# Kernel optimization log

Hardware: AMD Instinct MI355X
Metric: run time of the kernel (lower is better)

The kernel has to match this reference:

```python
import jax, jax.numpy as jnp
import numpy as np

B, S, E, P, H, F = 4, 4096, 256, 32, 8, 1024
DH = E // H
LN_EPS = 1e-5


def setup_inputs() -> dict:
    key = jax.random.key(0)
    ks = jax.random.split(key, 12)
    dt = jnp.float32
    return {
        "src": jax.random.normal(ks[0], (B, S, E), dt),
        "pos_embed": jax.random.normal(ks[1], (B, P, S), dt),
        # learnable positional transform (pos_linear: P -> P)
        "Wpos": jax.random.normal(ks[2], (P, P), dt) * (1.0 / np.sqrt(P)),
        "bpos": jnp.zeros((P,), dt),
        # RBF kernel hyperparameters (ScaleKernel(RBFKernel)) -- positive scalars
        "lengthscale": jnp.full((), 2.0, dt),
        "outputscale": jnp.full((), 1.0, dt),
        # value / output projections of multihead attention
        "Wv": jax.random.normal(ks[3], (E, E), dt) * (1.0 / np.sqrt(E)),
        "bv": jnp.zeros((E,), dt),
        "Wo": jax.random.normal(ks[4], (E, E), dt) * (1.0 / np.sqrt(E)),
        "bo": jnp.zeros((E,), dt),
        # feed-forward
        "W1": jax.random.normal(ks[5], (F, E), dt) * (1.0 / np.sqrt(E)),
        "b1": jnp.zeros((F,), dt),
        "W2": jax.random.normal(ks[6], (E, F), dt) * (1.0 / np.sqrt(F)),
        "b2": jnp.zeros((E,), dt),
        # layer norms
        "ln1_g": jnp.ones((E,), dt), "ln1_b": jnp.zeros((E,), dt),
        "ln2_g": jnp.ones((E,), dt), "ln2_b": jnp.zeros((E,), dt),
    }


def _layer_norm(x, g, b):
    mu = jnp.mean(x, -1, keepdims=True)
    var = jnp.mean(jnp.square(x - mu), -1, keepdims=True)
    return (x - mu) * jax.lax.rsqrt(var + LN_EPS) * g + b


def _rbf_scores(x, lengthscale, outputscale):
    # x: [B, S, P] -> scaled RBF kernel matrix [B, S, S]
    xs = x / lengthscale
    sq = jnp.sum(xs * xs, axis=-1)  # [B, S]
    d2 = sq[:, :, None] + sq[:, None, :] - 2.0 * jnp.einsum('bsp,btp->bst', xs, xs)
    d2 = jnp.maximum(d2, 0.0)
    return outputscale * jnp.exp(-0.5 * d2)


def reference(src, pos_embed, Wpos, bpos, lengthscale, outputscale,
              Wv, bv, Wo, bo, W1, b1, W2, b2, ln1_g, ln1_b, ln2_g, ln2_b):
    b, s, e = src.shape
    # learnable positional transform: [B,P,S] -> [B,S,P] -> linear -> back
    pe = jnp.einsum('bps,op->bos', pos_embed, Wpos) + bpos[None, :, None]  # [B,P,S]
    # GP-kernel attention scores over sequence positions
    scores = _rbf_scores(pe.transpose(0, 2, 1), lengthscale, outputscale)  # [B,S,S]
    attn = jax.nn.softmax(scores, axis=-1)
    # value projection, per-head weighted sum (scores shared across heads)
    v = (src @ Wv.T + bv).reshape(b, s, H, DH)
    ctx = jnp.einsum('bqk,bkhd->bqhd', attn, v).reshape(b, s, e)
    attn_out = ctx @ Wo.T + bo
    x = _layer_norm(src + attn_out, ln1_g, ln1_b)
    ff = jax.nn.relu(x @ W1.T + b1) @ W2.T + b2
    return _layer_norm(x + ff, ln2_g, ln2_b)
```

## Files before the change

### kernel.cpp

```cpp
#include <hip/hip_runtime.h>
#include <stdint.h>

#define BN 4
#define SN 4096
#define EN 256
#define PN 32
#define FN 1024
#define BS (BN*SN)
#define PAUG 64

typedef uint16_t bf16_t;
typedef short v4s  __attribute__((ext_vector_type(4)));
typedef short v8s  __attribute__((ext_vector_type(8)));
typedef __bf16 bf16x8 __attribute__((ext_vector_type(8)));
typedef float v4f   __attribute__((ext_vector_type(4)));
typedef float v16f  __attribute__((ext_vector_type(16)));

#define MFMA16(a,b,c) __builtin_amdgcn_mfma_f32_16x16x32_bf16(a,b,c,0,0,0)
#define MFMA32(a,b,c) __builtin_amdgcn_mfma_f32_32x32x16_bf16(a,b,c,0,0,0)

__device__ __forceinline__ float b2f(bf16_t x){
    uint32_t u = ((uint32_t)x) << 16; float f; __builtin_memcpy(&f, &u, 4); return f;
}
__device__ __forceinline__ bf16_t f2b(float f){
    uint32_t u; __builtin_memcpy(&u, &f, 4);
    u += 0x7FFFu + ((u >> 16) & 1u);
    return (bf16_t)(u >> 16);
}
__device__ __forceinline__ bf16x8 ldb8(const bf16_t* p){
    v8s r = *(const v8s*)p; return __builtin_bit_cast(bf16x8, r);
}
__device__ __forceinline__ bf16x8 ldb8u(const bf16_t* p){
    v4s lo = *(const v4s*)p;
    v4s hi = *(const v4s*)(p + 4);
    v8s r = __builtin_shufflevector(lo, hi, 0,1,2,3,4,5,6,7);
    return __builtin_bit_cast(bf16x8, r);
}
__device__ __forceinline__ float ldsc(const float* p){ return *p; }
__device__ __forceinline__ float ldsc(const bf16_t* p){ return b2f(*p); }
__device__ __forceinline__ void stsc(float* p, float v){ *p = v; }
__device__ __forceinline__ void stsc(bf16_t* p, float v){ *p = f2b(v); }

#if __has_builtin(__builtin_amdgcn_exp2f)
__device__ __forceinline__ float fexp2(float x){ return __builtin_amdgcn_exp2f(x); }
#else
__device__ __forceinline__ float fexp2(float x){ return exp2f(x); }
#endif

#if __has_builtin(__builtin_amdgcn_cvt_pk_bf16_f32)
typedef __bf16 bf16x2 __attribute__((ext_vector_type(2)));
__device__ __forceinline__ uint32_t pkbf16(float a, float b){
    bf16x2 r = __builtin_amdgcn_cvt_pk_bf16_f32(a, b);
    return __builtin_bit_cast(uint32_t, r);
}
#else
__device__ __forceinline__ uint32_t pkbf16(float a, float b){
    return (uint32_t)f2b(a) | ((uint32_t)f2b(b) << 16);
}
#endif

typedef const __attribute__((address_space(1))) uint32_t* glds_gp;
typedef __attribute__((address_space(3))) uint32_t* glds_lp;
__device__ __forceinline__ void glds16(const bf16_t* g, bf16_t* l){
    __builtin_amdgcn_global_load_lds((glds_gp)g, (glds_lp)l, 16, 0, 0);
}

__global__ __launch_bounds__(256) void prep_kernel(
    const float* __restrict__ src, bf16_t* __restrict__ srcb,
    const float* __restrict__ Wv, bf16_t* __restrict__ Wvb,
    const float* __restrict__ Wo, bf16_t* __restrict__ Wob,
    const float* __restrict__ W1, bf16_t* __restrict__ W1b,
    const float* __restrict__ W2, bf16_t* __restrict__ W2b,
    const float* __restrict__ pos, const float* __restrict__ Wp,
    const float* __restrict__ bp,  const float* __restrict__ lsp,
    bf16_t* __restrict__ xk, bf16_t* __restrict__ xq)
{
    __shared__ float Wsh[PN*PN];
    __shared__ float bsh[PN];
    int bid = blockIdx.x;
    int tid = threadIdx.x;

    if (bid < 4736){
        const float* sp; bf16_t* dp; int off;
        if (bid < 4096){ sp = src; dp = srcb; off = (bid*256 + tid)*4; }
        else {
            int i = ((bid - 4096)*256 + tid)*4;
            if      (i <  65536){ sp=Wv; dp=Wvb; off=i; }
            else if (i < 131072){
                int idx = i - 65536;
                float4 f = *(const float4*)(Wo + idx);
                v4s o;
                o.x = (short)f2b(f.x); o.y = (short)f2b(f.y);
                o.z = (short)f2b(f.z); o.w = (short)f2b(f.w);
                int n = idx >> 8, k = idx & 255;
                int dst = (((n>>4)*8 + (k>>5))*64 + (((k>>3)&3)*16 + (n&15)))*8 + (k&7);
                *(v4s*)(Wob + dst) = o;
                return;
            }
            else if (i < 393216){ sp=W1; dp=W1b; off=i-131072; }
            else                { sp=W2; dp=W2b; off=i-393216; }
        }
        float4 f = *(const float4*)(sp + off);
        v4s o;
        o.x = (short)f2b(f.x); o.y = (short)f2b(f.y);
        o.z = (short)f2b(f.z); o.w = (short)f2b(f.w);
        *(v4s*)(dp + off) = o;
        return;
    }

    int pb = bid - 4736;
    int b  = pb >> 4;
    int s  = (pb & 15)*256 + tid;

    for (int i = tid; i < PN*PN; i += 256) Wsh[i] = Wp[i];
    if (tid < PN) bsh[tid] = bp[tid];
    __syncthreads();

    float inv_ls = 1.0f / lsp[0];
    const float c1f = 1.4426950408889634f;

    float col[PN];
    #pragma unroll
    for (int p = 0; p < PN; p++) col[p] = pos[((size_t)b*PN + p)*SN + s];

    uint16_t xb[PN], qb[PN];
    float sq = 0.f;
    #pragma unroll 4
    for (int o = 0; o < PN; o++){
        float pe = bsh[o];
        #pragma unroll
        for (int p = 0; p < PN; p++) pe += col[p] * Wsh[o*PN + p];
        float pv = pe * inv_ls;
        uint16_t h = f2b(pv);
        xb[o] = h;
        qb[o] = f2b(c1f * pv);
        float xr = b2f(h);
        sq += xr * xr;
    }

    size_t base = ((size_t)b*SN + s) * PAUG;
    v8s pk[8];
    #pragma unroll
    for (int c = 0; c < 4; c++)
        #pragma unroll
        for (int j = 0; j < 8; j++) ((short*)&pk[c])[j] = (short)xb[c*8 + j];
    #pragma unroll
    for (int c = 4; c < 8; c++)
        #pragma unroll
        for (int j = 0; j < 8; j++) ((short*)&pk[c])[j] = 0;
    ((short*)&pk[4])[0] = (short)f2b(-0.5f * sq);
    ((short*)&pk[4])[1] = (short)0x3F80;
    #pragma unroll
    for (int c = 0; c < 8; c++) *(v8s*)(xk + base + c*8) = pk[c];

    #pragma unroll
    for (int c = 0; c < 4; c++)
        #pragma unroll
        for (int j = 0; j < 8; j++) ((short*)&pk[c])[j] = (short)qb[c*8 + j];
    ((short*)&pk[4])[0] = (short)f2b(c1f);
    ((short*)&pk[4])[1] = (short)f2b(-0.5f * sq * c1f);
    #pragma unroll
    for (int c = 0; c < 8; c++) *(v8s*)(xq + base + c*8) = pk[c];
}

template<int EPI, typename OutT>
__global__ __launch_bounds__(256) void gemm_t(
    const bf16_t* __restrict__ A, const bf16_t* __restrict__ W,
    const float* __restrict__ bias, OutT* __restrict__ out,
    bf16_t* __restrict__ vt, int N, int K)
{
    __shared__ __align__(16) bf16_t At[2][4096];
    __shared__ __align__(16) bf16_t Wt[2][4096];
    int tid = threadIdx.x;
    int lane = tid & 63, wv = tid >> 6, col = lane & 15, quad = lane >> 4;
    int m0 = blockIdx.x * 64, n0 = blockIdx.y * 64;
    int nck = K >> 6;

    int srow = tid >> 3;
    int spc  = (tid & 7) ^ (srow & 7);
    const bf16_t* asrc = A + (size_t)(m0 + srow)*K + spc*8;
    const bf16_t* wsrc = W + (size_t)(n0 + srow)*K + spc*8;

    v4f acc[4];
    #pragma unroll
    for (int t = 0; t < 4; t++) acc[t] = (v4f){0.f,0.f,0.f,0.f};

    glds16(asrc, &At[0][tid*8]);
    glds16(asrc + (size_t)32*K, &At[0][2048 + tid*8]);
    glds16(wsrc, &Wt[0][tid*8]);
    glds16(wsrc + (size_t)32*K, &Wt[0][2048 + tid*8]);
    __syncthreads();

    for (int c = 0; c < nck; c++){
        int cb = c & 1;
        if (c + 1 < nck){
            glds16(asrc + (c+1)*64, &At[cb^1][tid*8]);
            glds16(asrc + (size_t)32*K + (c+1)*64, &At[cb^1][2048 + tid*8]);
            glds16(wsrc + (c+1)*64, &Wt[cb^1][tid*8]);
            glds16(wsrc + (size_t)32*K + (c+1)*64, &Wt[cb^1][2048 + tid*8]);
        }
        #pragma unroll
        for (int kc = 0; kc < 2; kc++){
            int pc = ((kc*4 + quad) ^ (col & 7)) * 8;
            bf16x8 a = ldb8(&At[cb][(wv*16 + col)*64 + pc]);
            #pragma unroll
            for (int t = 0; t < 4; t++){
                bf16x8 b = ldb8(&Wt[cb][(t*16 + col)*64 + pc]);
                acc[t] = MFMA16(a, b, acc[t]);
            }
        }
        __syncthreads();
    }

    float bfv[4];
    #pragma unroll
    for (int t = 0; t < 4; t++) bfv[t] = bias[n0 + t*16 + col];

    if constexpr (EPI == 3){
        __shared__ uint16_t Tsh[64*74];
        #pragma unroll
        for (int r = 0; r < 4; r++)
            #pragma unroll
            for (int t = 0; t < 4; t++)
                Tsh[(wv*16 + quad*4 + r)*74 + t*16 + col] = f2b(acc[t][r] + bfv[t]);
        __syncthreads();
        int e = tid & 63, sc = tid >> 6;
        int b = m0 >> 12;
        int sbat = m0 & (SN-1);
        int eb   = (n0 + e) >> 5;
        int l31e = (n0 + e) & 31;
        int k16  = (sbat >> 4) + sc;
        v8s p0, p1;
        #pragma unroll
        for (int i = 0; i < 8; i++) ((short*)&p0)[i] = (short)Tsh[(sc*16 + i)*74 + e];
        #pragma unroll
        for (int i = 0; i < 8; i++) ((short*)&p1)[i] = (short)Tsh[(sc*16 + 8 + i)*74 + e];
        bf16_t* dst = vt + ((((size_t)b*8 + eb)*256 + k16)*64 + l31e)*8;
        *(v8s*)dst = p0;
        *(v8s*)(dst + 256) = p1;
    } else {
        #pragma unroll
        for (int r = 0; r < 4; r++){
            int row = m0 + wv*16 + quad*4 + r;
            #pragma unroll
            for (int t = 0; t < 4; t++){
                float y = acc[t][r] + bfv[t];
                if constexpr (EPI == 1) y = fmaxf(y, 0.f);
                stsc(out + (size_t)row*N + n0 + t*16 + col, y);
            }
        }
    }
}

__global__ __launch_bounds__(512) void ffn_ln_kernel(
    const bf16_t* __restrict__ x,  const bf16_t* __restrict__ W1b,
    const float* __restrict__ b1,  const bf16_t* __restrict__ W2b,
    const float* __restrict__ b2,  const float* __restrict__ gamma,
    const float* __restrict__ beta, float* __restrict__ out)
{
    __shared__ __align__(16) bf16_t W1c[2][16384];
    __shared__ __align__(16) bf16_t W2c[2][16384];
    __shared__ __align__(16) bf16_t Hs[64*68];
    __shared__ float b1sh[1024];
    __shared__ float lnb[2][64][2];

    int tid  = threadIdx.x;
    int lane = tid & 63;
    int wv   = tid >> 6;
    int col  = lane & 15;
    int quad = lane >> 4;
    int mw   = wv >> 1;
    int nw   = wv & 1;
    int m0   = blockIdx.x * 64;

    b1sh[tid]       = b1[tid];
    b1sh[512 + tid] = b1[512 + tid];

    const bf16_t* xrow = x + (size_t)(m0 + mw*16 + col)*EN + quad*8;
    bf16x8 xr[8];
    #pragma unroll
    for (int kk = 0; kk < 8; kk++) xr[kk] = ldb8(xrow + kk*32);

    float b2v[8], gv[8], bev[8];
    #pragma unroll
    for (int t2 = 0; t2 < 8; t2++){
        int nn = nw*128 + t2*16 + col;
        b2v[t2] = b2[nn]; gv[t2] = gamma[nn]; bev[t2] = beta[nn];
    }

    v4f acc[8];
    #pragma unroll
    for (int t2 = 0; t2 < 8; t2++) acc[t2] = (v4f){0.f,0.f,0.f,0.f};

    int wr  = tid >> 3;
    int pp  = tid & 7;
    int swz = (pp ^ (wr & 7)) * 8;

    #pragma unroll
    for (int s = 0; s < 4; s++)
        glds16(W1b + (size_t)wr*256 + s*64 + swz, &W1c[0][s*4096 + tid*8]);
    #pragma unroll
    for (int s2 = 0; s2 < 4; s2++)
        glds16(W2b + (size_t)(s2*64 + wr)*1024 + swz, &W2c[0][s2*4096 + tid*8]);

    #pragma unroll 1
    for (int c = 0; c < 16; c++){
        int par = c & 1;
        if (c < 15){
            #pragma unroll
            for (int s = 0; s < 4; s++)
                glds16(W1b + (size_t)((c+1)*64 + wr)*256 + s*64 + swz,
                       &W1c[par^1][s*4096 + tid*8]);
            #pragma unroll
            for (int s2 = 0; s2 < 4; s2++)
                glds16(W2b + (size_t)(s2*64 + wr)*1024 + (c+1)*64 + swz,
                       &W2c[par^1][s2*4096 + tid*8]);
            asm volatile("s_waitcnt vmcnt(8)" ::: "memory");
        } else {
            asm volatile("s_waitcnt vmcnt(0)" ::: "memory");
        }
        __builtin_amdgcn_s_barrier();
        __builtin_amdgcn_sched_barrier(0);

        v4f hacc[2];
        hacc[0] = (v4f){0.f,0.f,0.f,0.f};
        hacc[1] = (v4f){0.f,0.f,0.f,0.f};
        #pragma unroll
        for (int kk = 0; kk < 8; kk++){
            #pragma unroll
            for (int t = 0; t < 2; t++){
                int hl = nw*32 + t*16 + col;
                bf16x8 b = ldb8(&W1c[par][(kk>>1)*4096 + hl*64
                                 + ((((kk&1)*4 + quad) ^ (hl & 7))*8)]);
                hacc[t] = MFMA16(xr[kk], b, hacc[t]);
            }
        }
        #pragma unroll
        for (int t = 0; t < 2; t++){
            float bb = b1sh[c*64 + nw*32 + t*16 + col];
            #pragma unroll
            for (int r = 0; r < 4; r++){
                float h = fmaxf(hacc[t][r] + bb, 0.f);
                Hs[(mw*16 + quad*4 + r)*68 + nw*32 + t*16 + col] = f2b(h);
            }
        }
        asm volatile("s_waitcnt lgkmcnt(0)" ::: "memory");
        __builtin_amdgcn_s_barrier();
        __builtin_amdgcn_sched_barrier(0);

        #pragma unroll
        for (int kk2 = 0; kk2 < 2; kk2++){
            bf16x8 a2 = ldb8u(&Hs[(mw*16 + col)*68 + kk2*32 + quad*8]);
            #pragma unroll
            for (int t2 = 0; t2 < 8; t2++){
                int nn = nw*128 + t2*16 + col;
                bf16x8 bfr = ldb8(&W2c[par][(nn>>6)*4096 + (nn&63)*64
                                  + ((((kk2*4 + quad) ^ (col & 7)))*8)]);
                acc[t2] = MFMA16(a2, bfr, acc[t2]);
            }
        }
        asm volatile("s_waitcnt lgkmcnt(0)" ::: "memory");
        __builtin_amdgcn_s_barrier();
    }

    float v[8][4];
    float s1[4], s2[4];
    #pragma unroll
    for (int r = 0; r < 4; r++){ s1[r] = 0.f; s2[r] = 0.f; }
    #pragma unroll
    for (int r = 0; r < 4; r++){
        int row = m0 + mw*16 + quad*4 + r;
        #pragma unroll
        for (int t2 = 0; t2 < 8; t2++){
            int nn = nw*128 + t2*16 + col;
            float xv = acc[t2][r] + b2v[t2] + b2f(x[(size_t)row*EN + nn]);
            v[t2][r] = xv; s1[r] += xv; s2[r] += xv*xv;
        }
    }
    #pragma unroll
    for (int r = 0; r < 4; r++){
        #pragma unroll
        for (int m = 1; m <= 8; m <<= 1){
            s1[r] += __shfl_xor(s1[r], m);
            s2[r] += __shfl_xor(s2[r], m);
        }
    }
    if (col == 0){
        #pragma unroll
        for (int r = 0; r < 4; r++){
            int rl = mw*16 + quad*4 + r;
            lnb[nw][rl][0] = s1[r];
            lnb[nw][rl][1] = s2[r];
        }
    }
    __syncthreads();
    #pragma unroll
    for (int r = 0; r < 4; r++){
        int rl  = mw*16 + quad*4 + r;
        int row = m0 + rl;
        float S1 = lnb[0][rl][0] + lnb[1][rl][0];
        float S2 = lnb[0][rl][1] + lnb[1][rl][1];
        float mu = S1 * (1.f/256.f);
        float rs = rsqrtf(S2 * (1.f/256.f) - mu*mu + 1e-5f);
        #pragma unroll
        for (int t2 = 0; t2 < 8; t2++){
            int nn = nw*128 + t2*16 + col;
            out[(size_t)row*EN + nn] = (v[t2][r] - mu)*rs*gv[t2] + bev[t2];
        }
    }
}

__global__ __launch_bounds__(512, 2) void attn_kernel(
    const bf16_t* __restrict__ xk, const bf16_t* __restrict__ xq,
    const bf16_t* __restrict__ vf, const float* __restrict__ osp,
    const bf16_t* __restrict__ wof, const float* __restrict__ bo,
    const bf16_t* __restrict__ res, const float* __restrict__ gamma,
    const float* __restrict__ beta, bf16_t* __restrict__ out)
{
    __shared__ __align__(16) bf16_t Wtb[2][64*260];
    __shared__ __align__(16) bf16_t Qs[64*64];
    __shared__ __align__(16) bf16_t Osh[64*256];
    __shared__ float densh[8][64];
    __shared__ float dent[64];
    __shared__ float lnw[8][64][2];

    int tid  = threadIdx.x;
    int lane = tid & 63;
    int wv   = tid >> 6;
    int col  = lane & 15;
    int quad = lane >> 4;
    int l31  = lane & 31;
    int half = lane >> 5;

    int bid = blockIdx.x;
    int b   = (bid & 7) >> 1;
    int qi  = ((bid >> 3) << 1) | (bid & 1);
    int q0  = qi * 64;

    float k2 = 1.4426950408889634f * osp[0];

    const bf16_t* xkb = xk + (size_t)b * SN * PAUG;
    const bf16_t* xqb = xq + (size_t)b * SN * PAUG;
    const bf16_t* vfb = vf + (((size_t)b*8 + wv)*256)*512 + lane*8;

    {
        int qrow = tid >> 3;
        int qpc  = (tid & 7) ^ (qrow & 7);
        glds16(xqb + (size_t)(q0 + qrow)*PAUG + qpc*8, &Qs[tid*8]);
    }

    v16f acc[2];
    #pragma unroll
    for (int qg = 0; qg < 2; qg++)
        #pragma unroll
        for (int i = 0; i < 16; i++) acc[qg][i] = 0.f;
    float den[4] = {0.f, 0.f, 0.f, 0.f};
    const v4f zero = (v4f){0.f,0.f,0.f,0.f};

    bf16x8 kf[2][2];
    #pragma unroll
    for (int kg = 0; kg < 2; kg++)
        #pragma unroll
        for (int h = 0; h < 2; h++)
            kf[kg][h] = ldb8(xkb + (size_t)(wv*32 + kg*16 + col)*PAUG + h*32 + quad*8);

    __syncthreads();

    for (int c = 0; c < 16; c++){
        int cb = c & 1;
        bf16x8 vr[16];
        #pragma unroll
        for (int sk = 0; sk < 16; sk++)
            vr[sk] = ldb8(vfb + (size_t)(c*16 + sk)*512);

        #pragma unroll
        for (int qg = 0; qg < 2; qg++){
            #pragma unroll
            for (int g2 = 0; g2 < 2; g2++){
                int qr = qg*32 + g2*16 + col;
                bf16x8 qa = ldb8(&Qs[qr*64 + ((quad    ) ^ (col & 7))*8]);
                bf16x8 qb = ldb8(&Qs[qr*64 + ((4 + quad) ^ (col & 7))*8]);
                #pragma unroll
                for (int kg = 0; kg < 2; kg++){
                    v4f st = MFMA16(kf[kg][0], qa, zero);
                    st = MFMA16(kf[kg][1], qb, st);
                    #pragma unroll
                    for (int rp = 0; rp < 2; rp++){
                        float w0 = fexp2(fmaf(k2, fexp2(st[rp*2+0]), -k2));
                        float w1 = fexp2(fmaf(k2, fexp2(st[rp*2+1]), -k2));
                        den[qg*2+g2] += w0 + w1;
                        *(uint32_t*)&Wtb[cb][qr*260 + wv*32 + kg*16 + quad*4 + rp*2]
                            = pkbf16(w0, w1);
                    }
                }
            }
        }

        if (c + 1 < 16){
            #pragma unroll
            for (int kg = 0; kg < 2; kg++)
                #pragma unroll
                for (int h = 0; h < 2; h++)
                    kf[kg][h] = ldb8(xkb + (size_t)((c+1)*256 + wv*32 + kg*16 + col)*PAUG
                                     + h*32 + quad*8);
        }

        asm volatile("s_waitcnt lgkmcnt(0)" ::: "memory");
        __builtin_amdgcn_s_barrier();
        __builtin_amdgcn_sched_barrier(0);

        #pragma unroll
        for (int qg = 0; qg < 2; qg++){
            #pragma unroll
            for (int sk4 = 0; sk4 < 4; sk4++){
                bf16x8 af[4];
                #pragma unroll
                for (int j = 0; j < 4; j++)
                    af[j] = ldb8u(&Wtb[cb][(qg*32 + l31)*260 + (sk4*4 + j)*16 + half*8]);
                #pragma unroll
                for (int j = 0; j < 4; j++)
                    acc[qg] = MFMA32(af[j], vr[sk4*4 + j], acc[qg]);
            }
        }
    }

    bf16x8 wf0[8];
    #pragma unroll
    for (int kc = 0; kc < 8; kc++)
        wf0[kc] = ldb8(wof + (size_t)(((wv*2+0)*8 + kc)*64 + lane)*8);

    #pragma unroll
    for (int d = 0; d < 4; d++){
        den[d] += __shfl_xor(den[d], 16);
        den[d] += __shfl_xor(den[d], 32);
    }
    if (lane < 16){
        #pragma unroll
        for (int qg = 0; qg < 2; qg++)
            #pragma unroll
            for (int g2 = 0; g2 < 2; g2++)
                densh[wv][qg*32 + g2*16 + lane] = den[qg*2+g2];
    }
    __syncthreads();
    if (tid < 64){
        float s = 0.f;
        #pragma unroll
        for (int w = 0; w < 8; w++) s += densh[w][tid];
        dent[tid] = 1.f / s;
    }
    __syncthreads();

    #pragma unroll
    for (int qg = 0; qg < 2; qg++){
        #pragma unroll
        for (int rg = 0; rg < 16; rg++){
            int qrow = qg*32 + (rg & 3) + 8*(rg >> 2) + 4*half;
            int e = wv*32 + l31;
            int g = e >> 3;
            Osh[qrow*256 + ((g ^ (qrow & 7))*8) + (e & 7)] = f2b(acc[qg][rg] * dent[qrow]);
        }
    }
    __syncthreads();

    v4f y[4][2];
    #pragma unroll
    for (int qg = 0; qg < 4; qg++)
        #pragma unroll
        for (int t = 0; t < 2; t++) y[qg][t] = (v4f){0.f,0.f,0.f,0.f};

    #pragma unroll
    for (int kc = 0; kc < 8; kc++){
        bf16x8 b1 = ldb8(wof + (size_t)(((wv*2+1)*8 + kc)*64 + lane)*8);
        #pragma unroll
        for (int qg = 0; qg < 4; qg++){
            bf16x8 a = ldb8(&Osh[(qg*16 + col)*256 + (((kc*4 + quad) ^ (col & 7))*8)]);
            y[qg][0] = MFMA16(a, wf0[kc], y[qg][0]);
            y[qg][1] = MFMA16(a, b1, y[qg][1]);
        }
    }

    size_t growb = (size_t)b*SN + q0;
    float bo0 = bo[wv*32 + col], bo1 = bo[wv*32 + 16 + col];
    #pragma unroll
    for (int qg = 0; qg < 4; qg++){
        #pragma unroll
        for (int r = 0; r < 4; r++){
            int row = qg*16 + quad*4 + r;
            float x0 = y[qg][0][r] + bo0 + b2f(res[(growb + row)*EN + wv*32 + col]);
            float x1 = y[qg][1][r] + bo1 + b2f(res[(growb + row)*EN + wv*32 + 16 + col]);
            y[qg][0][r] = x0; y[qg][1][r] = x1;
            float s1 = x0 + x1, s2 = x0*x0 + x1*x1;
            #pragma unroll
            for (int m = 1; m <= 8; m <<= 1){
                s1 += __shfl_xor(s1, m);
                s2 += __shfl_xor(s2, m);
            }
            if (col == 0){
                lnw[wv][row][0] = s1;
                lnw[wv][row][1] = s2;
            }
        }
    }
    __syncthreads();

    float g0 = gamma[wv*32 + col],      g1v = gamma[wv*32 + 16 + col];
    float e0 = beta[wv*32 + col],       e1v = beta[wv*32 + 16 + col];
    #pragma unroll
    for (int qg = 0; qg < 4; qg++){
        #pragma unroll
        for (int r = 0; r < 4; r++){
            int row = qg*16 + quad*4 + r;
            float S1 = 0.f, S2 = 0.f;
            #pragma unroll
            for (int w = 0; w < 8; w++){ S1 += lnw[w][row][0]; S2 += lnw[w][row][1]; }
            float mu = S1 * (1.f/256.f);
            float rs = rsqrtf(S2 * (1.f/256.f) - mu*mu + 1e-5f);
            out[(growb + row)*EN + wv*32 + col]      = f2b((y[qg][0][r]-mu)*rs*g0 + e0);
            out[(growb + row)*EN + wv*32 + 16 + col] = f2b((y[qg][1][r]-mu)*rs*g1v + e1v);
        }
    }
}

extern "C" void kernel_launch(void* const* d_in, const int* in_sizes, int n_in,
                              void* d_out, int out_size, void* d_ws, size_t ws_size,
                              hipStream_t stream)
{
    (void)in_sizes; (void)n_in; (void)out_size; (void)ws_size;
    const float* src  = (const float*)d_in[0];
    const float* pos  = (const float*)d_in[1];
    const float* Wpos = (const float*)d_in[2];
    const float* bpos = (const float*)d_in[3];
    const float* ls   = (const float*)d_in[4];
    const float* os   = (const float*)d_in[5];
    const float* Wv   = (const float*)d_in[6];
    const float* bv   = (const float*)d_in[7];
    const float* Wo   = (const float*)d_in[8];
    const float* bo   = (const float*)d_in[9];
    const float* W1   = (const float*)d_in[10];
    const float* b1   = (const float*)d_in[11];
    const float* W2   = (const float*)d_in[12];
    const float* b2   = (const float*)d_in[13];
    const float* g1   = (const float*)d_in[14];
    const float* be1  = (const float*)d_in[15];
    const float* g2   = (const float*)d_in[16];
    const float* be2  = (const float*)d_in[17];

    char* w = (char*)d_ws;
    bf16_t* xkb  = (bf16_t*)(w);
    bf16_t* xqb  = (bf16_t*)(w + ( 2u<<20));
    bf16_t* Wvb  = (bf16_t*)(w + ( 4u<<20));
    bf16_t* Wob  = (bf16_t*)(w + ( 4u<<20) + (1u<<18));
    bf16_t* W1b  = (bf16_t*)(w + ( 5u<<20));
    bf16_t* W2b  = (bf16_t*)(w + ( 6u<<20));
    bf16_t* srcb = (bf16_t*)(w + ( 8u<<20));
    bf16_t* vtg  = (bf16_t*)(w + (16u<<20));
    bf16_t* xws  = (bf16_t*)(w + (24u<<20));

    prep_kernel<<<dim3(4800), 256, 0, stream>>>(
        src, srcb, Wv, Wvb, Wo, Wob, W1, W1b, W2, W2b,
        pos, Wpos, bpos, ls, xkb, xqb);

    gemm_t<3, bf16_t><<<dim3(BS/64, EN/64), 256, 0, stream>>>(
        srcb, Wvb, bv, (bf16_t*)nullptr, vtg, EN, EN);
    attn_kernel<<<dim3(256), 512, 0, stream>>>(
        xkb, xqb, vtg, os, Wob, bo, srcb, g1, be1, xws);
    ffn_ln_kernel<<<dim3(BS/64), 512, 0, stream>>>(
        xws, W1b, b1, W2b, b2, g2, be2, (float*)d_out);
}
```

Baseline: 224.1 us.

## Shrink FFN row tile to 32, drop double buffering, raise occupancy

The FFN+LayerNorm kernel now processes 32 rows per block instead of 64, splits the output columns over 4 waves instead of 2, and replaces the double-buffered weight staging in LDS with a single buffer loaded synchronously every chunk. LDS use drops by half and launch bounds request 4 blocks per CU, so more blocks can be resident and the grid doubles to fill more CUs. In exchange, each block re-streams the full W1/W2 weights for half as many rows, doubling total weight traffic, and global loads are no longer overlapped with compute inside a block. The design relies on other resident blocks to hide that latency.

```diff
diff --git a/kernel.cpp b/kernel.cpp
--- a/kernel.cpp
+++ b/kernel.cpp
@@ -252,26 +252,26 @@
     }
 }
 
-__global__ __launch_bounds__(512) void ffn_ln_kernel(
+__global__ __launch_bounds__(512, 4) void ffn_ln_kernel(
     const bf16_t* __restrict__ x,  const bf16_t* __restrict__ W1b,
     const float* __restrict__ b1,  const bf16_t* __restrict__ W2b,
     const float* __restrict__ b2,  const float* __restrict__ gamma,
     const float* __restrict__ beta, float* __restrict__ out)
 {
-    __shared__ __align__(16) bf16_t W1c[2][16384];
-    __shared__ __align__(16) bf16_t W2c[2][16384];
-    __shared__ __align__(16) bf16_t Hs[64*68];
+    __shared__ __align__(16) bf16_t W1c[16384];
+    __shared__ __align__(16) bf16_t W2c[16384];
+    __shared__ __align__(16) bf16_t Hs[32*68];
     __shared__ float b1sh[1024];
-    __shared__ float lnb[2][64][2];
+    __shared__ float lnb[4][32][2];
 
     int tid  = threadIdx.x;
     int lane = tid & 63;
     int wv   = tid >> 6;
     int col  = lane & 15;
     int quad = lane >> 4;
-    int mw   = wv >> 1;
-    int nw   = wv & 1;
-    int m0   = blockIdx.x * 64;
+    int mw   = wv >> 2;
+    int nw   = wv & 3;
+    int m0   = blockIdx.x * 32;
 
     b1sh[tid]       = b1[tid];
     b1sh[512 + tid] = b1[512 + tid];
@@ -281,69 +281,47 @@
     #pragma unroll
     for (int kk = 0; kk < 8; kk++) xr[kk] = ldb8(xrow + kk*32);
 
-    float b2v[8], gv[8], bev[8];
-    #pragma unroll
-    for (int t2 = 0; t2 < 8; t2++){
-        int nn = nw*128 + t2*16 + col;
+    float b2v[4], gv[4], bev[4];
+    #pragma unroll
+    for (int t2 = 0; t2 < 4; t2++){
+        int nn = nw*64 + t2*16 + col;
         b2v[t2] = b2[nn]; gv[t2] = gamma[nn]; bev[t2] = beta[nn];
     }
 
-    v4f acc[8];
-    #pragma unroll
-    for (int t2 = 0; t2 < 8; t2++) acc[t2] = (v4f){0.f,0.f,0.f,0.f};
+    v4f acc[4];
+    #pragma unroll
+    for (int t2 = 0; t2 < 4; t2++) acc[t2] = (v4f){0.f,0.f,0.f,0.f};
 
     int wr  = tid >> 3;
     int pp  = tid & 7;
     int swz = (pp ^ (wr & 7)) * 8;
 
-    #pragma unroll
-    for (int s = 0; s < 4; s++)
-        glds16(W1b + (size_t)wr*256 + s*64 + swz, &W1c[0][s*4096 + tid*8]);
-    #pragma unroll
-    for (int s2 = 0; s2 < 4; s2++)
-        glds16(W2b + (size_t)(s2*64 + wr)*1024 + swz, &W2c[0][s2*4096 + tid*8]);
-
     #pragma unroll 1
     for (int c = 0; c < 16; c++){
-        int par = c & 1;
-        if (c < 15){
-            #pragma unroll
-            for (int s = 0; s < 4; s++)
-                glds16(W1b + (size_t)((c+1)*64 + wr)*256 + s*64 + swz,
-                       &W1c[par^1][s*4096 + tid*8]);
-            #pragma unroll
-            for (int s2 = 0; s2 < 4; s2++)
-                glds16(W2b + (size_t)(s2*64 + wr)*1024 + (c+1)*64 + swz,
-                       &W2c[par^1][s2*4096 + tid*8]);
-            asm volatile("s_waitcnt vmcnt(8)" ::: "memory");
-        } else {
-            asm volatile("s_waitcnt vmcnt(0)" ::: "memory");
-        }
+        #pragma unroll
+        for (int s = 0; s < 4; s++)
+            glds16(W1b + (size_t)(c*64 + wr)*256 + s*64 + swz,
+                   &W1c[s*4096 + tid*8]);
+        #pragma unroll
+        for (int s2 = 0; s2 < 4; s2++)
+            glds16(W2b + (size_t)(s2*64 + wr)*1024 + c*64 + swz,
+                   &W2c[s2*4096 + tid*8]);
+        asm volatile("s_waitcnt vmcnt(0)" ::: "memory");
         __builtin_amdgcn_s_barrier();
         __builtin_amdgcn_sched_barrier(0);
 
-        v4f hacc[2];
-        hacc[0] = (v4f){0.f,0.f,0.f,0.f};
-        hacc[1] = (v4f){0.f,0.f,0.f,0.f};
+        int hl = nw*16 + col;
+        v4f hacc = (v4f){0.f,0.f,0.f,0.f};
         #pragma unroll
         for (int kk = 0; kk < 8; kk++){
-            #pragma unroll
-            for (int t = 0; t < 2; t++){
-                int hl = nw*32 + t*16 + col;
-                bf16x8 b = ldb8(&W1c[par][(kk>>1)*4096 + hl*64
-                                 + ((((kk&1)*4 + quad) ^ (hl & 7))*8)]);
-                hacc[t] = MFMA16(xr[kk], b, hacc[t]);
-            }
-        }
-        #pragma unroll
-        for (int t = 0; t < 2; t++){
-            float bb = b1sh[c*64 + nw*32 + t*16 + col];
-            #pragma unroll
-            for (int r = 0; r < 4; r++){
-                float h = fmaxf(hacc[t][r] + bb, 0.f);
-                Hs[(mw*16 + quad*4 + r)*68 + nw*32 + t*16 + col] = f2b(h);
-            }
-        }
+            bf16x8 b = ldb8(&W1c[(kk>>1)*4096 + hl*64
+                             + ((((kk&1)*4 + quad) ^ (hl & 7))*8)]);
+            hacc = MFMA16(xr[kk], b, hacc);
+        }
+        float bb = b1sh[c*64 + hl];
+        #pragma unroll
+        for (int r = 0; r < 4; r++)
+            Hs[(mw*16 + quad*4 + r)*68 + hl] = f2b(fmaxf(hacc[r] + bb, 0.f));
         asm volatile("s_waitcnt lgkmcnt(0)" ::: "memory");
         __builtin_amdgcn_s_barrier();
         __builtin_amdgcn_sched_barrier(0);
@@ -352,10 +330,10 @@
         for (int kk2 = 0; kk2 < 2; kk2++){
             bf16x8 a2 = ldb8u(&Hs[(mw*16 + col)*68 + kk2*32 + quad*8]);
             #pragma unroll
-            for (int t2 = 0; t2 < 8; t2++){
-                int nn = nw*128 + t2*16 + col;
-                bf16x8 bfr = ldb8(&W2c[par][(nn>>6)*4096 + (nn&63)*64
-                                  + ((((kk2*4 + quad) ^ (col & 7)))*8)]);
+            for (int t2 = 0; t2 < 4; t2++){
+                int nn = nw*64 + t2*16 + col;
+                bf16x8 bfr = ldb8(&W2c[(nn>>6)*4096 + (nn&63)*64
+                                  + (((kk2*4 + quad) ^ (col & 7))*8)]);
                 acc[t2] = MFMA16(a2, bfr, acc[t2]);
             }
         }
@@ -363,7 +341,7 @@
         __builtin_amdgcn_s_barrier();
     }
 
-    float v[8][4];
+    float v[4][4];
     float s1[4], s2[4];
     #pragma unroll
     for (int r = 0; r < 4; r++){ s1[r] = 0.f; s2[r] = 0.f; }
@@ -371,8 +349,8 @@
     for (int r = 0; r < 4; r++){
         int row = m0 + mw*16 + quad*4 + r;
         #pragma unroll
-        for (int t2 = 0; t2 < 8; t2++){
-            int nn = nw*128 + t2*16 + col;
+        for (int t2 = 0; t2 < 4; t2++){
+            int nn = nw*64 + t2*16 + col;
             float xv = acc[t2][r] + b2v[t2] + b2f(x[(size_t)row*EN + nn]);
             v[t2][r] = xv; s1[r] += xv; s2[r] += xv*xv;
         }
@@ -398,13 +376,13 @@
     for (int r = 0; r < 4; r++){
         int rl  = mw*16 + quad*4 + r;
         int row = m0 + rl;
-        float S1 = lnb[0][rl][0] + lnb[1][rl][0];
-        float S2 = lnb[0][rl][1] + lnb[1][rl][1];
+        float S1 = lnb[0][rl][0] + lnb[1][rl][0] + lnb[2][rl][0] + lnb[3][rl][0];
+        float S2 = lnb[0][rl][1] + lnb[1][rl][1] + lnb[2][rl][1] + lnb[3][rl][1];
         float mu = S1 * (1.f/256.f);
         float rs = rsqrtf(S2 * (1.f/256.f) - mu*mu + 1e-5f);
         #pragma unroll
-        for (int t2 = 0; t2 < 8; t2++){
-            int nn = nw*128 + t2*16 + col;
+        for (int t2 = 0; t2 < 4; t2++){
+            int nn = nw*64 + t2*16 + col;
             out[(size_t)row*EN + nn] = (v[t2][r] - mu)*rs*gv[t2] + bev[t2];
         }
     }
@@ -664,6 +642,6 @@
         srcb, Wvb, bv, (bf16_t*)nullptr, vtg, EN, EN);
     attn_kernel<<<dim3(256), 512, 0, stream>>>(
         xkb, xqb, vtg, os, Wob, bo, srcb, g1, be1, xws);
-    ffn_ln_kernel<<<dim3(BS/64), 512, 0, stream>>>(
+    ffn_ln_kernel<<<dim3(BS/32), 512, 0, stream>>>(
         xws, W1b, b1, W2b, b2, g2, be2, (float*)d_out);
 }
```

Result: no change. 226.3 us, median of 2 (+1.0%).
